# Performance work log

Hardware: AMD Instinct MI355X
Metric: run time of the kernel (lower is better)

Reference implementation:

```python
import jax, jax.numpy as jnp
import numpy as np

IGNORE_ID = -1
NEG_INF = -jnp.inf


def ctc_force_align(log_probs, ctc_label):
    """Viterbi forced alignment, vectorized over batch, scan over time.

    log_probs: [B, T, V] log-softmaxed CTC outputs (blank = 0).
    ctc_label: [B, L] int labels in [1, V).
    Returns align: [B, L] float32, begin frame (1-based, t+1) of each label.
    Assumes uniform lengths: input_len = T, target_len = L for every item
    (how the inputs are generated here).
    """
    B, T, V = log_probs.shape
    L = ctc_label.shape[1]
    N = 2 * L + 1  # CTC state lattice: blank,label,blank,...

    labels = jnp.zeros((B, N), dtype=ctc_label.dtype).at[:, 1::2].set(ctc_label)
    # per-state emission log-prob: [B, T, N]
    lab_b = jnp.broadcast_to(labels[:, None, :], (B, T, N))
    lp_states = jnp.take_along_axis(log_probs, lab_b, axis=2)

    idx = jnp.arange(N)
    ihalf = idx.astype(jnp.float32) / 2.0
    # labels[i] == labels[i-2] (False for i < 2)
    same_label = labels == jnp.concatenate(
        [jnp.full((B, 2), -1, labels.dtype), labels[:, :-2]], axis=1)
    two_way = (idx % 2 == 0)[None, :] | (idx == 1)[None, :] | same_label  # [B, N]

    ts = jnp.arange(T).astype(jnp.float32)
    # infeasible if i/2 > t or L - i/2 > T - t  (float division as in original)
    feas = ~((ihalf[None, :] > ts[:, None]) |
             (float(L) - ihalf[None, :] > float(T) - ts[:, None]))  # [T, N]

    a0 = jnp.where(idx[None, :] < 2, lp_states[:, 0, :], NEG_INF)  # [B, N]

    def shift(x, k):
        return jnp.pad(x, ((0, 0), (k, 0)), constant_values=NEG_INF)[:, :N]

    def step(a_prev, inputs):
        lp_t, feas_t = inputs  # [B, N], [N]
        p0, p1, p2 = a_prev, shift(a_prev, 1), shift(a_prev, 2)
        val_two = jnp.where(p0 > p1, idx, idx - 1)
        best0 = (p0 > p1) & (p0 > p2)
        best1 = (p1 > p0) & (p1 > p2)
        val_three = jnp.where(best0, idx, jnp.where(best1, idx - 1, idx - 2))
        val = jnp.where(idx[None, :] == 0, 0,
                        jnp.where(two_way, val_two, val_three))
        off = idx[None, :] - val
        a_sel = jnp.where(off == 0, p0, jnp.where(off == 1, p1, p2))
        a_new = jnp.where(feas_t[None, :], a_sel + lp_t, NEG_INF)
        v = jnp.where(feas_t[None, :], val, 0).astype(jnp.int32)
        return a_new, v

    lp_tb = jnp.moveaxis(lp_states, 1, 0)  # [T, B, N]
    a_final, v_all = jax.lax.scan(step, a0, (lp_tb[1:], feas[1:]))
    # v_all: [T-1, B, N] for t = 1 .. T-1
    v_all = jnp.moveaxis(v_all, 1, 0)  # [B, T-1, N]

    def backtrace(a_fin, v_seq):  # a_fin: [N], v_seq: [T-1, N]
        use_last = a_fin[N - 1] > a_fin[N - 2]
        pre0 = jnp.where(use_last, N - 1, N - 2)
        align0 = jnp.where((jnp.arange(L) == L - 1) & (~use_last),
                           float(T), 0.0).astype(jnp.float32)
        tp1 = jnp.arange(T - 1, 0, -1)  # t+1 values: T-1 .. 1
        lidx = jnp.arange(L)

        def bstep(carry, inp):
            pre, align = carry
            v_row, t1 = inp
            pre = v_row[pre]
            odd = (pre % 2) == 1
            align = jnp.where((lidx == pre // 2) & odd,
                              t1.astype(jnp.float32), align)
            return (pre, align), None

        (_, align), _ = jax.lax.scan(bstep, (pre0, align0), (v_seq[::-1], tp1))
        return align

    return jax.vmap(backtrace)(a_final, v_all)  # [B, L]


def setup_inputs() -> dict:
    key = jax.random.key(0)
    k0, k1, k2, k3, k4 = jax.random.split(key, 5)
    B, layers, L, T, V = 16, 6, 200, 1000, 5000
    ali_out = jax.random.uniform(k0, (B, layers, L + 1, T), dtype=jnp.float32)
    ali_beg = jax.random.randint(k1, (B, L), 0, T, dtype=jnp.int32)
    ali_end = jax.random.randint(k2, (B, L), 0, T, dtype=jnp.int32)
    enc_mask = jnp.zeros((B, T), dtype=bool)
    ctc_out = jax.random.normal(k3, (B, T, V), dtype=jnp.float32)
    ctc_label = jax.random.randint(k4, (B, L), 1, V, dtype=jnp.int32)
    ctc_len = jnp.full((B,), T, dtype=jnp.int32)
    return {"ali_out": ali_out, "ali_beg": ali_beg, "ali_end": ali_end,
            "enc_mask": enc_mask, "ctc_out": ctc_out,
            "ctc_label": ctc_label, "ctc_len": ctc_len}


def reference(ali_out, ali_beg, ali_end, enc_mask, ctc_out, ctc_label, ctc_len):
    B, layers, olen, ilen = ali_out.shape
    hlen = enc_mask.shape[1]  # == ilen == T
    # forced alignment on detached (stop-gradient) log-probs
    log_probs = jax.lax.stop_gradient(jax.nn.log_softmax(ctc_out, axis=2))
    ali = ctc_force_align(log_probs, ctc_label)  # [B, L] float32
    # expected position: matmul with pos_vec = [1..hlen], drop last output step
    pos = jnp.arange(1, hlen + 1, dtype=ali_out.dtype)
    ali_pos = jnp.einsum('bloi,i->blo', ali_out, pos)[:, :, :-1]  # [B, layers, L]
    ylens = jnp.sum(ali_beg != IGNORE_ID, axis=1)  # [B]
    mask = jnp.arange(olen - 1)[None, :] >= ylens[:, None]  # [B, L] pad mask
    total = (~mask).sum().astype(ali_out.dtype) * layers
    lat = jnp.where(mask[:, None, :], 0.0, ali_pos - ali[:, None, :])
    return (lat ** 2).sum() / total / hlen
```

## Files before the change

### kernel.cpp

```cpp
#include <hip/hip_runtime.h>
#include <hip/hip_bf16.h>
#include <math.h>

#define NEGINF (-INFINITY)

typedef float f32x4 __attribute__((ext_vector_type(4)));

__device__ __forceinline__ float wave_max_f(float m) {
#pragma unroll
  for (int d = 32; d > 0; d >>= 1) m = fmaxf(m, __shfl_xor(m, d, 64));
  return m;
}
__device__ __forceinline__ float wave_sum_f(float s) {
#pragma unroll
  for (int d = 32; d > 0; d >>= 1) s += __shfl_xor(s, d, 64);
  return s;
}
__device__ __forceinline__ int wave_sum_i(int s) {
#pragma unroll
  for (int d = 32; d > 0; d >>= 1) s += __shfl_xor(s, d, 64);
  return s;
}

__device__ __forceinline__ float dpp_wave_shr1(float x) {
  int r = __builtin_amdgcn_mov_dpp(__float_as_int(x), 0x138, 0xf, 0xf, true);
  return __int_as_float(r);
}
__device__ __forceinline__ float rdlane58(float x) {
  return __int_as_float(__builtin_amdgcn_readlane(__float_as_int(x), 58));
}

__global__ __launch_bounds__(256) void kA_lse_gather(
    const float* __restrict__ ctc_out, const int* __restrict__ ctc_label,
    float* __restrict__ lp, int B, int T, int V, int L, int LANES,
    int TPAD, int ROWF)
{
  extern __shared__ float shrow[];
  __shared__ float wred[4];
  int row = blockIdx.x;
  int b = row / T;
  int t = row - b * T;
  int tid = threadIdx.x;
  int w = tid >> 6;
  const float* x = ctc_out + (size_t)row * V;

  float m = NEGINF;
  int nf4 = V >> 2;
  for (int k = tid; k < nf4; k += 256) {
    float4 v = reinterpret_cast<const float4*>(x)[k];
    reinterpret_cast<float4*>(shrow)[k] = v;
    m = fmaxf(m, fmaxf(fmaxf(v.x, v.y), fmaxf(v.z, v.w)));
  }
  for (int k = (nf4 << 2) + tid; k < V; k += 256) {
    float v = x[k]; shrow[k] = v; m = fmaxf(m, v);
  }
  m = wave_max_f(m);
  if ((tid & 63) == 0) wred[w] = m;
  __syncthreads();
  float bm = fmaxf(fmaxf(wred[0], wred[1]), fmaxf(wred[2], wred[3]));
  __syncthreads();

  float s = 0.f;
  for (int k = tid; k < V; k += 256) s += __expf(shrow[k] - bm);
  s = wave_sum_f(s);
  if ((tid & 63) == 0) wred[w] = s;
  __syncthreads();
  float lse = bm + __logf(wred[0] + wred[1] + wred[2] + wred[3]);

  const int* lab = ctc_label + (size_t)b * L;
  float* dst = lp + ((size_t)b * TPAD + t) * ROWF;
  int nq = LANES * 4;
  for (int idx = tid; idx < nq; idx += 256) {
    int sl = idx >> 2, q = idx & 3;
    int jb = ((7 * sl) >> 1) + 1;
    int j = jb + q; if (j > L) j = L;
    int vi = lab[j - 1];
    if ((unsigned)vi >= (unsigned)V) vi = 0;
    dst[idx] = shrow[vi] - lse;
  }
  if (tid == 0) dst[nq] = shrow[0] - lse;
  for (int z = nq + 1 + tid; z < ROWF; z += 256) dst[z] = 0.f;
}

__global__ __launch_bounds__(64, 1) void kB_viterbi(
    const float* __restrict__ lp, const int* __restrict__ ctc_label,
    float* __restrict__ ali, int B, int T, int L, int TPAD, int ROWF)
{
  extern __shared__ float smemf[];
  const int N = 2 * L + 1;
  const int LANES = (N + 6) / 7;

  int b = blockIdx.x;
  int lane = threadIdx.x;
  const float* lpb = lp + (size_t)b * TPAD * ROWF;
  const int* lab = ctc_label + (size_t)b * L;
  int qlane = (lane < LANES) ? lane : LANES;

  int i0 = lane * 7;
  float a0v, a1v, a2v, a3v, a4v, a5v, a6v;
  float ainf0, ainf1, ainf2, ainf3, ainf4, ainf5, ainf6;
  {
    float ai[7];
#pragma unroll
    for (int s = 0; s < 7; ++s) {
      int i = i0 + s;
      bool valid = (i < N);
      bool odd = (i & 1) != 0;
      int li = (i - 1) >> 1;
      int myl = (odd && valid) ? lab[li] : 0;
      int pl  = (odd && valid && i >= 3) ? lab[li - 1] : -1;
      bool two = ((!odd) || (i == 1) || (myl == pl));
      ai[s] = two ? NEGINF : 0.f;
    }
    ainf0 = ai[0]; ainf1 = ai[1]; ainf2 = ai[2]; ainf3 = ai[3];
    ainf4 = ai[4]; ainf5 = ai[5]; ainf6 = ai[6];
  }
  bool pb0 = ((lane + 0) & 1) != 0;
  bool pb1 = ((lane + 1) & 1) != 0;
  bool pb2 = pb0, pb3 = pb1, pb4 = pb0, pb5 = pb1, pb6 = pb0;

  {
    f32x4 q00 = *reinterpret_cast<const f32x4*>(lpb + qlane * 4);
    float bl00 = lpb[LANES * 4];
    a0v = (i0 == 0) ? bl00 : NEGINF;
    a1v = NEGINF; a2v = NEGINF; a3v = NEGINF; a4v = NEGINF; a5v = NEGINF;
    a6v = NEGINF;
    if (i0 + 1 == 1) a1v = q00.x;
  }

  f32x4 rq0, rq1, rq2, rq3, rq4, rq5, rq6, rq7, rq8, rq9, rq10, rq11;
  unsigned* offu = (unsigned*)smemf;
  int wix = lane;

  asm volatile("s_waitcnt vmcnt(0) lgkmcnt(0)");
  __builtin_amdgcn_sched_barrier(0);

  unsigned long long base64 = (unsigned long long)lpb;
  unsigned voff = (unsigned)(qlane * 16) + 960u;

#define LOADQ(SL)                                                             \
  asm volatile("global_load_dwordx4 %0, %1, %2"                               \
               : "=v"(rq##SL) : "v"(voff), "s"(base64));                      \
  voff += 960u;

  LOADQ(1) LOADQ(2) LOADQ(3) LOADQ(4) LOADQ(5) LOADQ(6)
  LOADQ(7) LOADQ(8) LOADQ(9) LOADQ(10) LOADQ(11) LOADQ(0)

#define STF(s, P0, P1, P2, E, BL, ND, SH, LO, HI)                             \
  {                                                                           \
    float q2 = (P2) + ainf##s;                                                \
    float asel = fmaxf(fmaxf((P0), (P1)), q2);                                \
    unsigned t01 = ((P0) > (P1)) ? 0u : 1u;                                   \
    unsigned off = (asel == q2) ? 2u : t01;                                   \
    pack |= off << ((SH) + 2 * (s));                                          \
    float lps = pb##s ? (E) : (BL);                                           \
    ND = asel + lps;                                                          \
  }

#define STS(s, P0, P1, P2, E, BL, ND, SH, LO, HI)                             \
  {                                                                           \
    STF(s, P0, P1, P2, E, BL, ND, SH, LO, HI)                                 \
    bool feas = ((s) >= (LO)) && ((s) <= (HI));                               \
    ND = feas ? ND : NEGINF;                                                  \
  }

#define BODY2(SA, SB, M, SM)                                                  \
  {                                                                           \
    const int tt = tt0 + 2 * (M);                                             \
    int lo1 = 2 * (L - T + tt) - i0;                                          \
    int hi1 = 2 * tt - i0;                                                    \
    (void)lo1; (void)hi1;                                                     \
    asm volatile("s_waitcnt vmcnt(10)");                                      \
    __builtin_amdgcn_sched_barrier(0);                                        \
    float blcA = rdlane58(rq##SA.x);                                          \
    float blcB = rdlane58(rq##SB.x);                                          \
    unsigned pack = 0;                                                        \
    float m0, m1, m2, m3, m4, m5, m6;                                         \
    SM(5, a5v, a4v, a3v, rq##SA.z, blcA, m5, 0, lo1, hi1)                     \
    SM(6, a6v, a5v, a4v, rq##SA.w, blcA, m6, 0, lo1, hi1)                     \
    float t6m = dpp_wave_shr1(m6);                                            \
    float t5m = dpp_wave_shr1(m5);                                            \
    SM(0, a0v, t6, t5, rq##SA.x, blcA, m0, 0, lo1, hi1)                       \
    SM(1, a1v, a0v, t6, rq##SA.x, blcA, m1, 0, lo1, hi1)                      \
    SM(2, a2v, a1v, a0v, rq##SA.y, blcA, m2, 0, lo1, hi1)                     \
    SM(3, a3v, a2v, a1v, rq##SA.y, blcA, m3, 0, lo1, hi1)                     \
    SM(4, a4v, a3v, a2v, rq##SA.z, blcA, m4, 0, lo1, hi1)                     \
    t6m = (lane == 0) ? NEGINF : t6m;                                         \
    t5m = (lane == 0) ? NEGINF : t5m;                                         \
    float n0, n1, n2, n3, n4, n5, n6;                                         \
    SM(5, m5, m4, m3, rq##SB.z, blcB, n5, 14, lo1 + 2, hi1 + 2)               \
    SM(6, m6, m5, m4, rq##SB.w, blcB, n6, 14, lo1 + 2, hi1 + 2)               \
    float t6n = dpp_wave_shr1(n6);                                            \
    float t5n = dpp_wave_shr1(n5);                                            \
    SM(0, m0, t6m, t5m, rq##SB.x, blcB, n0, 14, lo1 + 2, hi1 + 2)             \
    SM(1, m1, m0, t6m, rq##SB.x, blcB, n1, 14, lo1 + 2, hi1 + 2)              \
    SM(2, m2, m1, m0, rq##SB.y, blcB, n2, 14, lo1 + 2, hi1 + 2)               \
    SM(3, m3, m2, m1, rq##SB.y, blcB, n3, 14, lo1 + 2, hi1 + 2)               \
    SM(4, m4, m3, m2, rq##SB.z, blcB, n4, 14, lo1 + 2, hi1 + 2)               \
    offu[wix] = pack;                                                         \
    wix += 64;                                                                \
    LOADQ(SA) LOADQ(SB)                                                       \
    a0v = n0; a1v = n1; a2v = n2; a3v = n3; a4v = n4; a5v = n5; a6v = n6;     \
    t6 = (lane == 0) ? NEGINF : t6n;                                          \
    t5 = (lane == 0) ? NEGINF : t5n;                                          \
  }

  float t6 = __shfl_up(a6v, 1, 64);
  float t5 = __shfl_up(a5v, 1, 64);
  if (lane == 0) { t6 = NEGINF; t5 = NEGINF; }

  int tt0 = 1;
  for (; tt0 + 12 <= T; tt0 += 12) {
    if (tt0 >= L && tt0 + 11 <= T - L) {
      BODY2(1, 2, 0, STF)  BODY2(3, 4, 1, STF)  BODY2(5, 6, 2, STF)
      BODY2(7, 8, 3, STF)  BODY2(9, 10, 4, STF) BODY2(11, 0, 5, STF)
    } else {
      BODY2(1, 2, 0, STS)  BODY2(3, 4, 1, STS)  BODY2(5, 6, 2, STS)
      BODY2(7, 8, 3, STS)  BODY2(9, 10, 4, STS) BODY2(11, 0, 5, STS)
    }
  }
#undef BODY2

  asm volatile("s_waitcnt vmcnt(0) lgkmcnt(0)" ::: "memory");
  __builtin_amdgcn_sched_barrier(0);
  asm volatile("" :: "v"(rq0), "v"(rq1), "v"(rq2), "v"(rq3));
  asm volatile("" :: "v"(rq4), "v"(rq5), "v"(rq6), "v"(rq7));
  asm volatile("" :: "v"(rq8), "v"(rq9), "v"(rq10), "v"(rq11));

  {
    unsigned pendpk = 0;
    for (int t = tt0; t < T; ++t) {
      f32x4 oc = *reinterpret_cast<const f32x4*>(lpb + (size_t)t * ROWF +
                                                 qlane * 4);
      float blcA = rdlane58(oc.x);
      int lo1 = 2 * (L - T + t) - i0;
      int hi1 = 2 * t - i0;
      unsigned pack = 0;
      float m0, m1, m2, m3, m4, m5, m6;
      STS(5, a5v, a4v, a3v, oc.z, blcA, m5, 0, lo1, hi1)
      STS(6, a6v, a5v, a4v, oc.w, blcA, m6, 0, lo1, hi1)
      float t6m = dpp_wave_shr1(m6);
      float t5m = dpp_wave_shr1(m5);
      STS(0, a0v, t6, t5, oc.x, blcA, m0, 0, lo1, hi1)
      STS(1, a1v, a0v, t6, oc.x, blcA, m1, 0, lo1, hi1)
      STS(2, a2v, a1v, a0v, oc.y, blcA, m2, 0, lo1, hi1)
      STS(3, a3v, a2v, a1v, oc.y, blcA, m3, 0, lo1, hi1)
      STS(4, a4v, a3v, a2v, oc.z, blcA, m4, 0, lo1, hi1)
      int bi = (t - 1) >> 1, sub = (t - 1) & 1;
      if (sub == 0) pendpk = pack; else pendpk |= pack << 14;
      if (sub == 1 || t == T - 1) offu[(size_t)bi * 64 + lane] = pendpk;
      a0v = m0; a1v = m1; a2v = m2; a3v = m3; a4v = m4; a5v = m5; a6v = m6;
      t6 = (lane == 0) ? NEGINF : t6m;
      t5 = (lane == 0) ? NEGINF : t5m;
    }
  }
#undef STS
#undef STF
#undef LOADQ

  int iN1 = N - 1, iN2 = N - 2;
  auto pick = [&](int sIdx) {
    float r = a0v;
    r = (sIdx == 1) ? a1v : r;
    r = (sIdx == 2) ? a2v : r;
    r = (sIdx == 3) ? a3v : r;
    r = (sIdx == 4) ? a4v : r;
    r = (sIdx == 5) ? a5v : r;
    r = (sIdx == 6) ? a6v : r;
    return r;
  };
  float vlast = __shfl(pick(iN1 % 7), iN1 / 7, 64);
  float vprev = __shfl(pick(iN2 % 7), iN2 / 7, 64);
  bool use_last = vlast > vprev;
  int pre = use_last ? iN1 : iN2;

  float al[4] = {0.f, 0.f, 0.f, 0.f};
  {
    int lbl = L - 1; int rr = lbl >> 6, ln = lbl & 63;
#pragma unroll
    for (int r = 0; r < 4; ++r)
      if (!use_last && rr == r && lane == ln) al[r] = (float)T;
  }

  const unsigned* ob = (const unsigned*)smemf;
  int t = T - 1;
  int g = pre / 7, mm = pre - g * 7;

#define CANDS(J, WA, WB, WC, GMV, THREE)                                      \
  {                                                                           \
    int lo = pcur - 2 * (J); if (lo < 0) lo = 0;                              \
    GMV = lo / 7;                                                             \
    int jr = ((J) < K) ? (J) : 0;                                             \
    const unsigned* rp = ob + (size_t)((t - 1 - jr) >> 1) * 64;               \
    WA = rp[GMV]; WB = rp[GMV + 1];                                           \
    if (THREE) WC = rp[GMV + 2]; else WC = WB;                                \
  }

#define DEC(J, WA, WB, WC, GMV)                                               \
  if ((J) < K) {                                                              \
    int gi = g - GMV;                                                         \
    unsigned w = (gi == 0) ? (WA) : ((gi == 1) ? (WB) : (WC));                \
    int sub = (t - 1 - (J)) & 1;                                              \
    unsigned off = (w >> (14 * sub + 2 * mm)) & 3u;                           \
    mm -= (int)off;                                                           \
    bool bor = mm < 0;                                                        \
    g = bor ? (g - 1) : g;                                                    \
    mm = bor ? (mm + 7) : mm;                                                 \
    int cur = 7 * g + mm;                                                     \
    if (cur & 1) {                                                            \
      int lbl = cur >> 1; int rr = lbl >> 6, ln = lbl & 63;                   \
      if (rr == 0 && lane == ln) al[0] = (float)(t - (J));                    \
      if (rr == 1 && lane == ln) al[1] = (float)(t - (J));                    \
      if (rr == 2 && lane == ln) al[2] = (float)(t - (J));                    \
      if (rr == 3 && lane == ln) al[3] = (float)(t - (J));                    \
    }                                                                         \
  }

  while (t >= 1) {
    int K = (t < 7) ? t : 7;
    int pcur = 7 * g + mm;
    unsigned w0 = ob[(size_t)((t - 1) >> 1) * 64 + g];
    unsigned w1a, w1b, w1c, w2a, w2b, w2c, w3a, w3b, w3c;
    unsigned w4a, w4b, w4c, w5a, w5b, w5c, w6a, w6b, w6c;
    int gm1, gm2, gm3, gm4, gm5, gm6;
    CANDS(1, w1a, w1b, w1c, gm1, 0)
    CANDS(2, w2a, w2b, w2c, gm2, 0)
    CANDS(3, w3a, w3b, w3c, gm3, 0)
    CANDS(4, w4a, w4b, w4c, gm4, 1)
    CANDS(5, w5a, w5b, w5c, gm5, 1)
    CANDS(6, w6a, w6b, w6c, gm6, 1)
    int gm0 = g;
    DEC(0, w0, w0, w0, gm0)
    DEC(1, w1a, w1b, w1c, gm1)
    DEC(2, w2a, w2b, w2c, gm2)
    DEC(3, w3a, w3b, w3c, gm3)
    DEC(4, w4a, w4b, w4c, gm4)
    DEC(5, w5a, w5b, w5c, gm5)
    DEC(6, w6a, w6b, w6c, gm6)
    t -= K;
  }
#undef DEC
#undef CANDS

#pragma unroll
  for (int r = 0; r < 4; ++r) {
    int l = lane + 64 * r;
    if (l < L) ali[(size_t)b * L + l] = al[r];
  }
}

__global__ __launch_bounds__(256) void kC_rows(
    const float* __restrict__ ali_out, const float* __restrict__ ali,
    const int* __restrict__ ali_beg, float* __restrict__ partials,
    int B, int layers, int L, int T)
{
  __shared__ float ps[4];
  int wid = threadIdx.x >> 6, lane = threadIdx.x & 63;
  int row = blockIdx.x * 4 + wid;
  int nrows = B * layers * L;
  float val = 0.f;
  if (row < nrows) {
    int o = row % L;
    int bl = row / L;
    int layer = bl % layers;
    int b = bl / layers;
    const float* x = ali_out + ((size_t)(b * layers + layer) * (L + 1) + o) * T;
    float s = 0.f;
    if ((T & 3) == 0) {
      int nf4 = T >> 2;
      for (int k = lane; k < nf4; k += 64) {
        float4 v = reinterpret_cast<const float4*>(x)[k];
        float base = (float)(4 * k);
        s += v.x * (base + 1.f) + v.y * (base + 2.f) +
             v.z * (base + 3.f) + v.w * (base + 4.f);
      }
    } else {
      for (int k = lane; k < T; k += 64) s += x[k] * (float)(k + 1);
    }
    s = wave_sum_f(s);
    int cnt = 0;
    for (int l = lane; l < L; l += 64)
      cnt += (ali_beg[(size_t)b * L + l] != -1) ? 1 : 0;
    cnt = wave_sum_i(cnt);
    if (lane == 0) {
      float lat = (o >= cnt) ? 0.f : (s - ali[(size_t)b * L + o]);
      val = lat * lat;
    }
  }
  if (lane == 0) ps[wid] = val;
  __syncthreads();
  if (threadIdx.x == 0) partials[blockIdx.x] = ps[0] + ps[1] + ps[2] + ps[3];
}

__global__ __launch_bounds__(256) void kD_final(
    const float* __restrict__ partials, int nparts,
    const int* __restrict__ ali_beg, int BL, int layers, int T,
    float* __restrict__ out)
{
  __shared__ float wred[4];
  __shared__ int wcnt[4];
  int tid = threadIdx.x, w = tid >> 6;
  float s = 0.f;
  for (int k = tid; k < nparts; k += 256) s += partials[k];
  s = wave_sum_f(s);
  int c = 0;
  for (int k = tid; k < BL; k += 256) c += (ali_beg[k] != -1) ? 1 : 0;
  c = wave_sum_i(c);
  if ((tid & 63) == 0) { wred[w] = s; wcnt[w] = c; }
  __syncthreads();
  if (tid == 0) {
    float ss = wred[0] + wred[1] + wred[2] + wred[3];
    float total = (float)(wcnt[0] + wcnt[1] + wcnt[2] + wcnt[3]) * (float)layers;
    out[0] = ss / total / (float)T;
  }
}

extern "C" void kernel_launch(void* const* d_in, const int* in_sizes, int n_in,
                              void* d_out, int out_size, void* d_ws, size_t ws_size,
                              hipStream_t stream)
{
  const float* ali_out   = (const float*)d_in[0];
  const int*   ali_beg   = (const int*)d_in[1];
  const float* ctc_out   = (const float*)d_in[4];
  const int*   ctc_label = (const int*)d_in[5];

  int B = in_sizes[6];
  int L = in_sizes[1] / B;
  int T = in_sizes[3] / B;
  int V = (int)((long long)in_sizes[4] / ((long long)B * T));
  int layers = (int)((long long)in_sizes[0] / ((long long)B * (L + 1) * T));

  int N = 2 * L + 1;
  int LANES = (N + 6) / 7;
  int ROWF = LANES * 4 + 8;
  int TPAD = T + 64;

  float* lp = (float*)d_ws;
  float* ali = lp + (size_t)B * TPAD * ROWF;
  float* partials = ali + (size_t)B * L;
  int nrows = B * layers * L;
  int gridC = (nrows + 3) / 4;

  size_t shA = (size_t)V * sizeof(float);
  hipLaunchKernelGGL(kA_lse_gather, dim3(B * T), dim3(256), shA, stream,
                     ctc_out, ctc_label, lp, B, T, V, L, LANES, TPAD, ROWF);

  size_t shB = (size_t)(T >> 1) * 256;
  hipFuncSetAttribute(reinterpret_cast<const void*>(kB_viterbi),
                      hipFuncAttributeMaxDynamicSharedMemorySize, (int)shB);
  hipLaunchKernelGGL(kB_viterbi, dim3(B), dim3(64), shB, stream,
                     lp, ctc_label, ali, B, T, L, TPAD, ROWF);

  hipLaunchKernelGGL(kC_rows, dim3(gridC), dim3(256), 0, stream,
                     ali_out, ali, ali_beg, partials, B, layers, L, T);

  hipLaunchKernelGGL(kD_final, dim3(1), dim3(256), 0, stream,
                     partials, gridC, ali_beg, B * L, layers, T, (float*)d_out);
}
```

Before: 413.8 us.

## Restructure Viterbi emission layout into fixed 256-float rows with separate blank array

The per-timestep emission buffer becomes a fixed 256-float quad layout plus a separate blank log-prob array, so the Viterbi kernel no longer needs a readlane broadcast for the blank value. It also issues a separate blank load per step, shortens the prefetch depth from 12 to 8 steps, and splits the feasibility masking into low-only and high-only variants to trim per-state compares. A new kernel copies the labels into the workspace, which adds an extra launch. The deeper-to-shallower prefetch and extra load instructions could expose more memory latency in the serial recurrence.

```diff
diff --git a/kernel.cpp b/kernel.cpp
--- a/kernel.cpp
+++ b/kernel.cpp
@@ -26,14 +26,11 @@
   int r = __builtin_amdgcn_mov_dpp(__float_as_int(x), 0x138, 0xf, 0xf, true);
   return __int_as_float(r);
 }
-__device__ __forceinline__ float rdlane58(float x) {
-  return __int_as_float(__builtin_amdgcn_readlane(__float_as_int(x), 58));
-}
 
 __global__ __launch_bounds__(256) void kA_lse_gather(
     const float* __restrict__ ctc_out, const int* __restrict__ ctc_label,
-    float* __restrict__ lp, int B, int T, int V, int L, int LANES,
-    int TPAD, int ROWF)
+    float* __restrict__ lpsQuad, float* __restrict__ blankArr,
+    int B, int T, int V, int L, int TPAD)
 {
   extern __shared__ float shrow[];
   __shared__ float wred[4];
@@ -68,38 +65,42 @@
   float lse = bm + __logf(wred[0] + wred[1] + wred[2] + wred[3]);
 
   const int* lab = ctc_label + (size_t)b * L;
-  float* dst = lp + ((size_t)b * TPAD + t) * ROWF;
-  int nq = LANES * 4;
-  for (int idx = tid; idx < nq; idx += 256) {
-    int sl = idx >> 2, q = idx & 3;
-    int jb = ((7 * sl) >> 1) + 1;
-    int j = jb + q; if (j > L) j = L;
-    int vi = lab[j - 1];
+  float* dq = lpsQuad + ((size_t)b * TPAD + t) * 256;
+  {
+    int l = tid >> 2, c = tid & 3;
+    int i_s = 7 * l + 2 * c + ((l & 1) ? 0 : 1);
+    int j = (i_s - 1) >> 1;
+    if (j >= L) j = L - 1;
+    if (j < 0) j = 0;
+    int vi = lab[j];
     if ((unsigned)vi >= (unsigned)V) vi = 0;
-    dst[idx] = shrow[vi] - lse;
-  }
-  if (tid == 0) dst[nq] = shrow[0] - lse;
-  for (int z = nq + 1 + tid; z < ROWF; z += 256) dst[z] = 0.f;
+    dq[tid] = shrow[vi] - lse;
+  }
+  if (tid == 0) blankArr[(size_t)b * TPAD + t] = shrow[0] - lse;
 }
 
 __global__ __launch_bounds__(64, 1) void kB_viterbi(
-    const float* __restrict__ lp, const int* __restrict__ ctc_label,
-    float* __restrict__ ali, int B, int T, int L, int TPAD, int ROWF)
+    const float* __restrict__ lpsQuad, const float* __restrict__ blankArr,
+    float* __restrict__ ali, int B, int T, int L, int TPAD)
 {
   extern __shared__ float smemf[];
   const int N = 2 * L + 1;
-  const int LANES = (N + 6) / 7;
 
   int b = blockIdx.x;
   int lane = threadIdx.x;
-  const float* lpb = lp + (size_t)b * TPAD * ROWF;
-  const int* lab = ctc_label + (size_t)b * L;
-  int qlane = (lane < LANES) ? lane : LANES;
+  const float* lpq = lpsQuad + (size_t)b * TPAD * 256;
+  const float* blk = blankArr + (size_t)b * TPAD;
 
   int i0 = lane * 7;
   float a0v, a1v, a2v, a3v, a4v, a5v, a6v;
   float ainf0, ainf1, ainf2, ainf3, ainf4, ainf5, ainf6;
   {
+    const int* lab = (const int*)nullptr;
+    (void)lab;
+  }
+  {
+    const int* lab2 = (const int*)(blankArr + (size_t)B * TPAD) +
+                      (size_t)b * L;
     float ai[7];
 #pragma unroll
     for (int s = 0; s < 7; ++s) {
@@ -107,8 +108,8 @@
       bool valid = (i < N);
       bool odd = (i & 1) != 0;
       int li = (i - 1) >> 1;
-      int myl = (odd && valid) ? lab[li] : 0;
-      int pl  = (odd && valid && i >= 3) ? lab[li - 1] : -1;
+      int myl = (odd && valid) ? lab2[li] : 0;
+      int pl  = (odd && valid && i >= 3) ? lab2[li - 1] : -1;
       bool two = ((!odd) || (i == 1) || (myl == pl));
       ai[s] = two ? NEGINF : 0.f;
     }
@@ -120,48 +121,58 @@
   bool pb2 = pb0, pb3 = pb1, pb4 = pb0, pb5 = pb1, pb6 = pb0;
 
   {
-    f32x4 q00 = *reinterpret_cast<const f32x4*>(lpb + qlane * 4);
-    float bl00 = lpb[LANES * 4];
+    f32x4 q00 = *reinterpret_cast<const f32x4*>(lpq + lane * 4);
+    float bl00 = blk[0];
     a0v = (i0 == 0) ? bl00 : NEGINF;
     a1v = NEGINF; a2v = NEGINF; a3v = NEGINF; a4v = NEGINF; a5v = NEGINF;
     a6v = NEGINF;
-    if (i0 + 1 == 1) a1v = q00.x;
-  }
-
-  f32x4 rq0, rq1, rq2, rq3, rq4, rq5, rq6, rq7, rq8, rq9, rq10, rq11;
+    if (lane == 0) a1v = q00.x;
+  }
+
+  f32x4 rq0, rq1, rq2, rq3, rq4, rq5, rq6, rq7;
+  float rb0, rb1, rb2, rb3, rb4, rb5, rb6, rb7;
   unsigned* offu = (unsigned*)smemf;
   int wix = lane;
 
   asm volatile("s_waitcnt vmcnt(0) lgkmcnt(0)");
   __builtin_amdgcn_sched_barrier(0);
 
-  unsigned long long base64 = (unsigned long long)lpb;
-  unsigned voff = (unsigned)(qlane * 16) + 960u;
+  unsigned long long baseQ = (unsigned long long)lpq;
+  unsigned long long baseB = (unsigned long long)blk;
+  unsigned voffQ = (unsigned)(lane * 16) + 1024u;
+  unsigned voffB = 4u;
 
 #define LOADQ(SL)                                                             \
   asm volatile("global_load_dwordx4 %0, %1, %2"                               \
-               : "=v"(rq##SL) : "v"(voff), "s"(base64));                      \
-  voff += 960u;
-
-  LOADQ(1) LOADQ(2) LOADQ(3) LOADQ(4) LOADQ(5) LOADQ(6)
-  LOADQ(7) LOADQ(8) LOADQ(9) LOADQ(10) LOADQ(11) LOADQ(0)
-
-#define STF(s, P0, P1, P2, E, BL, ND, SH, LO, HI)                             \
+               : "=v"(rq##SL) : "v"(voffQ), "s"(baseQ));                      \
+  voffQ += 1024u;
+#define LOADB(SL)                                                             \
+  asm volatile("global_load_dword %0, %1, %2"                                 \
+               : "=v"(rb##SL) : "v"(voffB), "s"(baseB));                      \
+  voffB += 4u;
+
+  LOADQ(0) LOADB(0) LOADQ(1) LOADB(1) LOADQ(2) LOADB(2) LOADQ(3) LOADB(3)
+  LOADQ(4) LOADB(4) LOADQ(5) LOADB(5) LOADQ(6) LOADB(6) LOADQ(7) LOADB(7)
+
+#define STF(s, P0, P1, P2, QC, BL, ND, PK, LO, HI)                            \
   {                                                                           \
     float q2 = (P2) + ainf##s;                                                \
     float asel = fmaxf(fmaxf((P0), (P1)), q2);                                \
     unsigned t01 = ((P0) > (P1)) ? 0u : 1u;                                   \
     unsigned off = (asel == q2) ? 2u : t01;                                   \
-    pack |= off << ((SH) + 2 * (s));                                          \
-    float lps = pb##s ? (E) : (BL);                                           \
+    PK |= off << (2 * (s));                                                   \
+    float lps = pb##s ? (QC) : (BL);                                          \
     ND = asel + lps;                                                          \
   }
-
-#define STS(s, P0, P1, P2, E, BL, ND, SH, LO, HI)                             \
+#define STS_HI(s, P0, P1, P2, QC, BL, ND, PK, LO, HI)                         \
   {                                                                           \
-    STF(s, P0, P1, P2, E, BL, ND, SH, LO, HI)                                 \
-    bool feas = ((s) >= (LO)) && ((s) <= (HI));                               \
-    ND = feas ? ND : NEGINF;                                                  \
+    STF(s, P0, P1, P2, QC, BL, ND, PK, LO, HI)                                \
+    ND = ((s) <= (HI)) ? ND : NEGINF;                                         \
+  }
+#define STS_LO(s, P0, P1, P2, QC, BL, ND, PK, LO, HI)                         \
+  {                                                                           \
+    STF(s, P0, P1, P2, QC, BL, ND, PK, LO, HI)                                \
+    ND = ((s) >= (LO)) ? ND : NEGINF;                                         \
   }
 
 #define BODY2(SA, SB, M, SM)                                                  \
@@ -170,36 +181,34 @@
     int lo1 = 2 * (L - T + tt) - i0;                                          \
     int hi1 = 2 * tt - i0;                                                    \
     (void)lo1; (void)hi1;                                                     \
-    asm volatile("s_waitcnt vmcnt(10)");                                      \
+    asm volatile("s_waitcnt vmcnt(12)");                                      \
     __builtin_amdgcn_sched_barrier(0);                                        \
-    float blcA = rdlane58(rq##SA.x);                                          \
-    float blcB = rdlane58(rq##SB.x);                                          \
-    unsigned pack = 0;                                                        \
+    unsigned packA = 0, packB = 0;                                            \
     float m0, m1, m2, m3, m4, m5, m6;                                         \
-    SM(5, a5v, a4v, a3v, rq##SA.z, blcA, m5, 0, lo1, hi1)                     \
-    SM(6, a6v, a5v, a4v, rq##SA.w, blcA, m6, 0, lo1, hi1)                     \
+    SM(5, a5v, a4v, a3v, rq##SA.z, rb##SA, m5, packA, lo1, hi1)               \
+    SM(6, a6v, a5v, a4v, rq##SA.w, rb##SA, m6, packA, lo1, hi1)               \
     float t6m = dpp_wave_shr1(m6);                                            \
     float t5m = dpp_wave_shr1(m5);                                            \
-    SM(0, a0v, t6, t5, rq##SA.x, blcA, m0, 0, lo1, hi1)                       \
-    SM(1, a1v, a0v, t6, rq##SA.x, blcA, m1, 0, lo1, hi1)                      \
-    SM(2, a2v, a1v, a0v, rq##SA.y, blcA, m2, 0, lo1, hi1)                     \
-    SM(3, a3v, a2v, a1v, rq##SA.y, blcA, m3, 0, lo1, hi1)                     \
-    SM(4, a4v, a3v, a2v, rq##SA.z, blcA, m4, 0, lo1, hi1)                     \
+    SM(0, a0v, t6, t5, rq##SA.x, rb##SA, m0, packA, lo1, hi1)                 \
+    SM(1, a1v, a0v, t6, rq##SA.x, rb##SA, m1, packA, lo1, hi1)                \
+    SM(2, a2v, a1v, a0v, rq##SA.y, rb##SA, m2, packA, lo1, hi1)               \
+    SM(3, a3v, a2v, a1v, rq##SA.y, rb##SA, m3, packA, lo1, hi1)               \
+    SM(4, a4v, a3v, a2v, rq##SA.z, rb##SA, m4, packA, lo1, hi1)               \
     t6m = (lane == 0) ? NEGINF : t6m;                                         \
     t5m = (lane == 0) ? NEGINF : t5m;                                         \
     float n0, n1, n2, n3, n4, n5, n6;                                         \
-    SM(5, m5, m4, m3, rq##SB.z, blcB, n5, 14, lo1 + 2, hi1 + 2)               \
-    SM(6, m6, m5, m4, rq##SB.w, blcB, n6, 14, lo1 + 2, hi1 + 2)               \
+    SM(5, m5, m4, m3, rq##SB.z, rb##SB, n5, packB, lo1 + 2, hi1 + 2)          \
+    SM(6, m6, m5, m4, rq##SB.w, rb##SB, n6, packB, lo1 + 2, hi1 + 2)          \
     float t6n = dpp_wave_shr1(n6);                                            \
     float t5n = dpp_wave_shr1(n5);                                            \
-    SM(0, m0, t6m, t5m, rq##SB.x, blcB, n0, 14, lo1 + 2, hi1 + 2)             \
-    SM(1, m1, m0, t6m, rq##SB.x, blcB, n1, 14, lo1 + 2, hi1 + 2)              \
-    SM(2, m2, m1, m0, rq##SB.y, blcB, n2, 14, lo1 + 2, hi1 + 2)               \
-    SM(3, m3, m2, m1, rq##SB.y, blcB, n3, 14, lo1 + 2, hi1 + 2)               \
-    SM(4, m4, m3, m2, rq##SB.z, blcB, n4, 14, lo1 + 2, hi1 + 2)               \
-    offu[wix] = pack;                                                         \
+    SM(0, m0, t6m, t5m, rq##SB.x, rb##SB, n0, packB, lo1 + 2, hi1 + 2)        \
+    SM(1, m1, m0, t6m, rq##SB.x, rb##SB, n1, packB, lo1 + 2, hi1 + 2)         \
+    SM(2, m2, m1, m0, rq##SB.y, rb##SB, n2, packB, lo1 + 2, hi1 + 2)          \
+    SM(3, m3, m2, m1, rq##SB.y, rb##SB, n3, packB, lo1 + 2, hi1 + 2)          \
+    SM(4, m4, m3, m2, rq##SB.z, rb##SB, n4, packB, lo1 + 2, hi1 + 2)          \
+    offu[wix] = packA | (packB << 14);                                        \
     wix += 64;                                                                \
-    LOADQ(SA) LOADQ(SB)                                                       \
+    LOADQ(SA) LOADB(SA) LOADQ(SB) LOADB(SB)                                   \
     a0v = n0; a1v = n1; a2v = n2; a3v = n3; a4v = n4; a5v = n5; a6v = n6;     \
     t6 = (lane == 0) ? NEGINF : t6n;                                          \
     t5 = (lane == 0) ? NEGINF : t5n;                                          \
@@ -210,13 +219,16 @@
   if (lane == 0) { t6 = NEGINF; t5 = NEGINF; }
 
   int tt0 = 1;
-  for (; tt0 + 12 <= T; tt0 += 12) {
-    if (tt0 >= L && tt0 + 11 <= T - L) {
-      BODY2(1, 2, 0, STF)  BODY2(3, 4, 1, STF)  BODY2(5, 6, 2, STF)
-      BODY2(7, 8, 3, STF)  BODY2(9, 10, 4, STF) BODY2(11, 0, 5, STF)
+  for (; tt0 + 8 <= T; tt0 += 8) {
+    if (tt0 >= L && tt0 + 7 <= T - L) {
+      BODY2(0, 1, 0, STF)  BODY2(2, 3, 1, STF)
+      BODY2(4, 5, 2, STF)  BODY2(6, 7, 3, STF)
+    } else if (tt0 < L) {
+      BODY2(0, 1, 0, STS_HI) BODY2(2, 3, 1, STS_HI)
+      BODY2(4, 5, 2, STS_HI) BODY2(6, 7, 3, STS_HI)
     } else {
-      BODY2(1, 2, 0, STS)  BODY2(3, 4, 1, STS)  BODY2(5, 6, 2, STS)
-      BODY2(7, 8, 3, STS)  BODY2(9, 10, 4, STS) BODY2(11, 0, 5, STS)
+      BODY2(0, 1, 0, STS_LO) BODY2(2, 3, 1, STS_LO)
+      BODY2(4, 5, 2, STS_LO) BODY2(6, 7, 3, STS_LO)
     }
   }
 #undef BODY2
@@ -225,27 +237,29 @@
   __builtin_amdgcn_sched_barrier(0);
   asm volatile("" :: "v"(rq0), "v"(rq1), "v"(rq2), "v"(rq3));
   asm volatile("" :: "v"(rq4), "v"(rq5), "v"(rq6), "v"(rq7));
-  asm volatile("" :: "v"(rq8), "v"(rq9), "v"(rq10), "v"(rq11));
+  asm volatile("" :: "v"(rb0), "v"(rb1), "v"(rb2), "v"(rb3));
+  asm volatile("" :: "v"(rb4), "v"(rb5), "v"(rb6), "v"(rb7));
 
   {
     unsigned pendpk = 0;
     for (int t = tt0; t < T; ++t) {
-      f32x4 oc = *reinterpret_cast<const f32x4*>(lpb + (size_t)t * ROWF +
-                                                 qlane * 4);
-      float blcA = rdlane58(oc.x);
+      f32x4 oc = *reinterpret_cast<const f32x4*>(lpq + (size_t)t * 256 +
+                                                 lane * 4);
+      float bl = blk[t];
       int lo1 = 2 * (L - T + t) - i0;
       int hi1 = 2 * t - i0;
+      (void)hi1;
       unsigned pack = 0;
       float m0, m1, m2, m3, m4, m5, m6;
-      STS(5, a5v, a4v, a3v, oc.z, blcA, m5, 0, lo1, hi1)
-      STS(6, a6v, a5v, a4v, oc.w, blcA, m6, 0, lo1, hi1)
+      STS_LO(5, a5v, a4v, a3v, oc.z, bl, m5, pack, lo1, hi1)
+      STS_LO(6, a6v, a5v, a4v, oc.w, bl, m6, pack, lo1, hi1)
       float t6m = dpp_wave_shr1(m6);
       float t5m = dpp_wave_shr1(m5);
-      STS(0, a0v, t6, t5, oc.x, blcA, m0, 0, lo1, hi1)
-      STS(1, a1v, a0v, t6, oc.x, blcA, m1, 0, lo1, hi1)
-      STS(2, a2v, a1v, a0v, oc.y, blcA, m2, 0, lo1, hi1)
-      STS(3, a3v, a2v, a1v, oc.y, blcA, m3, 0, lo1, hi1)
-      STS(4, a4v, a3v, a2v, oc.z, blcA, m4, 0, lo1, hi1)
+      STS_LO(0, a0v, t6, t5, oc.x, bl, m0, pack, lo1, hi1)
+      STS_LO(1, a1v, a0v, t6, oc.x, bl, m1, pack, lo1, hi1)
+      STS_LO(2, a2v, a1v, a0v, oc.y, bl, m2, pack, lo1, hi1)
+      STS_LO(3, a3v, a2v, a1v, oc.y, bl, m3, pack, lo1, hi1)
+      STS_LO(4, a4v, a3v, a2v, oc.z, bl, m4, pack, lo1, hi1)
       int bi = (t - 1) >> 1, sub = (t - 1) & 1;
       if (sub == 0) pendpk = pack; else pendpk |= pack << 14;
       if (sub == 1 || t == T - 1) offu[(size_t)bi * 64 + lane] = pendpk;
@@ -254,9 +268,11 @@
       t5 = (lane == 0) ? NEGINF : t5m;
     }
   }
-#undef STS
+#undef STS_LO
+#undef STS_HI
 #undef STF
 #undef LOADQ
+#undef LOADB
 
   int iN1 = N - 1, iN2 = N - 2;
   auto pick = [&](int sIdx) {
@@ -415,6 +431,13 @@
   }
 }
 
+__global__ __launch_bounds__(256) void kL_copy(
+    const int* __restrict__ src, int* __restrict__ dst, int n)
+{
+  int i = blockIdx.x * 256 + threadIdx.x;
+  if (i < n) dst[i] = src[i];
+}
+
 extern "C" void kernel_launch(void* const* d_in, const int* in_sizes, int n_in,
                               void* d_out, int out_size, void* d_ws, size_t ws_size,
                               hipStream_t stream)
@@ -430,26 +453,28 @@
   int V = (int)((long long)in_sizes[4] / ((long long)B * T));
   int layers = (int)((long long)in_sizes[0] / ((long long)B * (L + 1) * T));
 
-  int N = 2 * L + 1;
-  int LANES = (N + 6) / 7;
-  int ROWF = LANES * 4 + 8;
-  int TPAD = T + 64;
-
-  float* lp = (float*)d_ws;
-  float* ali = lp + (size_t)B * TPAD * ROWF;
+  int TPAD = T + 16;
+
+  float* lpsQuad = (float*)d_ws;
+  float* blankArr = lpsQuad + (size_t)B * TPAD * 256;
+  int* labCopy = (int*)(blankArr + (size_t)B * TPAD);
+  float* ali = (float*)(labCopy + (size_t)B * L);
   float* partials = ali + (size_t)B * L;
   int nrows = B * layers * L;
   int gridC = (nrows + 3) / 4;
 
+  hipLaunchKernelGGL(kL_copy, dim3((B * L + 255) / 256), dim3(256), 0, stream,
+                     ctc_label, labCopy, B * L);
+
   size_t shA = (size_t)V * sizeof(float);
   hipLaunchKernelGGL(kA_lse_gather, dim3(B * T), dim3(256), shA, stream,
-                     ctc_out, ctc_label, lp, B, T, V, L, LANES, TPAD, ROWF);
+                     ctc_out, ctc_label, lpsQuad, blankArr, B, T, V, L, TPAD);
 
   size_t shB = (size_t)(T >> 1) * 256;
   hipFuncSetAttribute(reinterpret_cast<const void*>(kB_viterbi),
                       hipFuncAttributeMaxDynamicSharedMemorySize, (int)shB);
   hipLaunchKernelGGL(kB_viterbi, dim3(B), dim3(64), shB, stream,
-                     lp, ctc_label, ali, B, T, L, TPAD, ROWF);
+                     lpsQuad, blankArr, ali, B, T, L, TPAD);
 
   hipLaunchKernelGGL(kC_rows, dim3(gridC), dim3(256), 0, stream,
                      ali_out, ali, ali_beg, partials, B, layers, L, T);
```

Result: no change. 411.3 us (-0.6%).
